# Kernel tuning notes

Hardware: AMD Instinct MI355X
Metric: run time of the kernel (lower is better)

## Reference

```python
import jax, jax.numpy as jnp
import numpy as np

K = 32  # kneighbors
BN_EPS = 1e-5


def setup_inputs() -> dict:
    key = jax.random.key(0)
    ks = jax.random.split(key, 8)
    B, N, S, C = 8, 4096, 1024, 64
    Cin = C + 6  # 70
    inp = {
        "xyz": jax.random.normal(ks[0], (B, N, 3), jnp.float32),
        "points": jax.random.normal(ks[1], (B, C, N), jnp.float32),
        "new_xyz": jax.random.normal(ks[2], (B, S, 3), jnp.float32),
        "W1": jax.random.normal(ks[3], (128, Cin), jnp.float32) / np.sqrt(Cin),
        "b1": jax.random.normal(ks[4], (128,), jnp.float32) * 0.01,
        "g1": jnp.ones((128,), jnp.float32),
        "be1": jnp.zeros((128,), jnp.float32),
        "W2": jax.random.normal(ks[5], (256, 128), jnp.float32) / np.sqrt(128),
        "b2": jax.random.normal(ks[6], (256,), jnp.float32) * 0.01,
        "g2": jnp.ones((256,), jnp.float32),
        "be2": jnp.zeros((256,), jnp.float32),
    }
    return inp


def _forward(xyz, points, new_xyz, W1, b1, g1, be1, W2, b2, g2, be2):
    B, S, _ = new_xyz.shape
    pts = jnp.transpose(points, (0, 2, 1))  # [B,N,C]
    # squared pairwise distances [B,S,N]
    sqd = (jnp.sum(new_xyz ** 2, -1)[:, :, None]
           + jnp.sum(xyz ** 2, -1)[:, None, :]
           - 2.0 * jnp.einsum('bsc,bnc->bsn', new_xyz, xyz))
    _, idx = jax.lax.top_k(-sqd, K)  # k smallest -> [B,S,K] int32
    gather = jax.vmap(lambda a, i: a[i])  # per-batch fancy gather
    gxyz = gather(xyz, idx)   # [B,S,K,3]
    gpts = gather(pts, idx)   # [B,S,K,C]
    q = jnp.broadcast_to(new_xyz[:, :, None, :], (B, S, K, 3))
    g = jnp.concatenate([gpts, gxyz, q], axis=-1)  # [B,S,K,C+6]
    x = jnp.transpose(g, (0, 3, 2, 1))  # [B,Cin,K,S]
    for W, b, gm, bt in ((W1, b1, g1, be1), (W2, b2, g2, be2)):
        x = jnp.einsum('oi,biks->boks', W, x) + b[None, :, None, None]
        mu = jnp.mean(x, axis=(0, 2, 3), keepdims=True)
        var = jnp.var(x, axis=(0, 2, 3), keepdims=True)  # biased, as torch BN train
        x = (x - mu) * jax.lax.rsqrt(var + BN_EPS)
        x = x * gm[None, :, None, None] + bt[None, :, None, None]
        x = jax.nn.relu(x)
    new_points = jnp.max(x, axis=2)  # [B,Cout,S]
    return new_xyz, new_points


def reference(xyz, points, new_xyz, W1, b1, g1, be1, W2, b2, g2, be2):
    return _forward(xyz, points, new_xyz, W1, b1, g1, be1, W2, b2, g2, be2)
```

## Files before the change

### kernel.cpp

```cpp
#include <hip/hip_runtime.h>
#include <stdint.h>

constexpr int Bn = 8, Nn = 4096, Sn = 1024, Cc = 64, KNN = 32, C1 = 128, C2 = 256;
constexpr int Qq = Bn * Sn;
constexpr int Mm = Qq * KNN;
constexpr int OUT_XYZ = Bn * Sn * 3;
constexpr float BNEPS = 1e-5f;
constexpr unsigned RSEL = 12;

constexpr size_t SZ_IDX  = (size_t)Qq * KNN * 4;
constexpr size_t SZ_PTST = (size_t)Bn * Nn * Cc * 2;
constexpr int    NB_MLP  = Mm / 64;
constexpr size_t SZ_P1   = (size_t)NB_MLP * 256 * 4;
constexpr size_t SZ_P2   = (size_t)NB_MLP * 512 * 4;
constexpr size_t OFF_IDX  = 0;
constexpr size_t OFF_PTST = OFF_IDX + SZ_IDX;
constexpr size_t OFF_P1   = OFF_PTST + SZ_PTST;
constexpr size_t OFF_P2   = OFF_P1 + SZ_P1;
constexpr size_t OFF_P1B  = OFF_P2 + SZ_P2;
constexpr size_t OFF_P2B  = OFF_P1B + (size_t)128 * 256 * 4;
constexpr size_t OFF_BN1  = OFF_P2B + (size_t)128 * 512 * 4;
constexpr size_t OFF_BN2  = OFF_BN1 + 1024;
constexpr size_t OFF_W2F  = OFF_BN2 + 2048;
constexpr size_t OFF_W1F  = OFF_W2F + (size_t)32768 * 2;
constexpr size_t OFF_Y1   = (OFF_W1F + (size_t)12288 * 2 + 255) & ~(size_t)255;
constexpr size_t OFF_MMX  = OFF_Y1 + (size_t)Mm * C1 * 2;
constexpr size_t OFF_MMN  = OFF_MMX + (size_t)Qq * C2 * 4;

typedef __attribute__((ext_vector_type(8))) __bf16 bf16x8;
typedef __attribute__((ext_vector_type(4))) float f32x4;

__device__ __forceinline__ unsigned short f2bf(float f) {
  unsigned u = __float_as_uint(f);
  u = u + 0x7FFFu + ((u >> 16) & 1u);
  return (unsigned short)(u >> 16);
}

__device__ __forceinline__ void agg_hist(unsigned* hist, unsigned bin, bool valid, int lane) {
  bool todo = valid;
  while (true) {
    unsigned long long bm = __ballot(todo);
    if (bm == 0ull) break;
    int first = __ffsll(bm) - 1;
    unsigned b = (unsigned)__shfl((int)bin, first);
    unsigned long long m = __ballot(todo && bin == b);
    if (lane == first) atomicAdd(&hist[b], (unsigned)__popcll(m));
    if (todo && bin == b) todo = false;
  }
}

__global__ __launch_bounds__(256) void k_knn(const float* __restrict__ xyz,
                                             const float* __restrict__ nxyz,
                                             int* __restrict__ idxout,
                                             const float* __restrict__ pts,
                                             const float* __restrict__ W1,
                                             const float* __restrict__ W2,
                                             unsigned short* __restrict__ ptsTbf,
                                             float* __restrict__ outdst,
                                             unsigned short* __restrict__ w1f,
                                             unsigned short* __restrict__ w2f) {
  int t = threadIdx.x;
  if (blockIdx.x >= (unsigned)Qq) {
    int blk = blockIdx.x - Qq;
    if (blk < 512) {
      __shared__ float tile[64][65];
      int b = blk >> 6, n0 = (blk & 63) * 64;
      int cl = t & 63, rw = t >> 6;
#pragma unroll
      for (int i = 0; i < 16; ++i) {
        int c = i * 4 + rw;
        tile[cl][c] = pts[((size_t)b * Cc + c) * Nn + n0 + cl];
      }
      __syncthreads();
#pragma unroll
      for (int i = 0; i < 16; ++i) {
        int nf = i * 4 + rw;
        ptsTbf[((size_t)b * Nn + n0 + nf) * Cc + cl] = f2bf(tile[nf][cl]);
      }
    } else if (blk < 608) {
      int i = t + (blk - 512) * 256;
      if (i < OUT_XYZ) outdst[i] = nxyz[i];
    } else if (blk < 656) {
      int u = t + (blk - 608) * 256;
      int j = u & 7, lane = (u >> 3) & 63, rest = u >> 9;
      int ks = rest % 3, nt = rest / 3;
      int ch = nt * 16 + (lane & 15);
      int k = ks * 32 + (lane >> 4) * 8 + j;
      w1f[u] = (k < 70) ? f2bf(W1[ch * 70 + k]) : (unsigned short)0;
    } else {
      int u = t + (blk - 656) * 256;
      int j = u & 7, lane = (u >> 3) & 63, ks = (u >> 9) & 3, ntile = u >> 11;
      int col = ntile * 16 + (lane & 15);
      int k = ks * 32 + (lane >> 4) * 8 + j;
      w2f[u] = f2bf(W2[col * C1 + k]);
    }
    return;
  }
  int q = blockIdx.x, b = q >> 10;
  int lane = t & 63, w = t >> 6;
  const float* xb = xyz + (size_t)b * Nn * 3;
  float qx = nxyz[q * 3 + 0], qy = nxyz[q * 3 + 1], qz = nxyz[q * 3 + 2];
  unsigned key[16];
  {
#pragma clang fp contract(off)
    float sqq = (qx * qx + qy * qy) + qz * qz;
#pragma unroll
    for (int i = 0; i < 16; ++i) {
      int p = t + (i << 8);
      float xl = xb[p * 3 + 0], yl = xb[p * 3 + 1], zl = xb[p * 3 + 2];
      float sqp = (xl * xl + yl * yl) + zl * zl;
      float dot = __builtin_fmaf(qz, zl, __builtin_fmaf(qy, yl, qx * xl));
      float d = (sqq + sqp) - 2.0f * dot;
      unsigned u = __float_as_uint(d);
      key[i] = (u & 0x80000000u) ? ~u : (u | 0x80000000u);
    }
  }
  __shared__ unsigned long long buf64[256];
  __shared__ unsigned hist[256];
  __shared__ unsigned hist2[256];
  __shared__ unsigned wsum[4];
  __shared__ unsigned sel_bin, sel_off, cnt, ovf, thrU, tieflag;
  __shared__ unsigned eqcnt;
  __shared__ int eqbuf[128];

  unsigned s0 = key[0], s1 = key[8];
  hist[t] = 0;
  hist2[t] = 0;
  if (t == 0) { cnt = 0; ovf = 0; thrU = 0xFFFFFFFFu; tieflag = 0; }
  __syncthreads();
  agg_hist(hist, s0 >> 24, true, lane);
  agg_hist(hist, s1 >> 24, true, lane);
  __syncthreads();
  {
    unsigned h = hist[t], v = h;
#pragma unroll
    for (int off = 1; off < 64; off <<= 1) {
      unsigned o = __shfl_up(v, off);
      if (lane >= off) v += o;
    }
    if (lane == 63) wsum[w] = v;
    __syncthreads();
    unsigned woff = 0;
    for (int ww = 0; ww < w; ++ww) woff += wsum[ww];
    v += woff;
    unsigned vex = v - h;
    if (vex < RSEL && RSEL <= v) { sel_bin = (unsigned)t; sel_off = RSEL - vex; }
    __syncthreads();
  }
  unsigned sbin = sel_bin, srem = sel_off;
  if ((s0 >> 24) == sbin) atomicAdd(&hist2[(s0 >> 16) & 255u], 1u);
  if ((s1 >> 24) == sbin) atomicAdd(&hist2[(s1 >> 16) & 255u], 1u);
  __syncthreads();
  {
    unsigned h = hist2[t], v = h;
#pragma unroll
    for (int off = 1; off < 64; off <<= 1) {
      unsigned o = __shfl_up(v, off);
      if (lane >= off) v += o;
    }
    if (lane == 63) wsum[w] = v;
    __syncthreads();
    unsigned woff = 0;
    for (int ww = 0; ww < w; ++ww) woff += wsum[ww];
    v += woff;
    unsigned vex = v - h;
    if (vex < srem && srem <= v) {
      unsigned p16 = (sbin << 8) | (unsigned)t;
      thrU = (p16 >= 0xFFFFu) ? 0xFFFFFFFFu : ((p16 + 1u) << 16);
    }
    __syncthreads();
  }
  unsigned U = thrU;
#pragma unroll
  for (int i = 0; i < 16; ++i) {
    bool take = key[i] < U;
    unsigned long long m = __ballot(take);
    if (m == 0ull) continue;
    unsigned base = 0;
    if (lane == 0) base = atomicAdd(&cnt, (unsigned)__popcll(m));
    base = (unsigned)__shfl((int)base, 0);
    if (take) {
      unsigned off = base + (unsigned)__popcll(m & ((1ull << lane) - 1ull));
      if (off < 256u)
        buf64[off] = ((unsigned long long)key[i] << 32) | (unsigned)(t + (i << 8));
      else
        ovf = 1;
    }
  }
  __syncthreads();
  unsigned ncnt = cnt;
  if (!ovf && ncnt >= (unsigned)KNN && ncnt <= 256u) {
    int nc = (int)ncnt;
    const unsigned* keyhw = reinterpret_cast<const unsigned*>(buf64);
    bool split = (nc <= 128);
    int cid = split ? (t & 127) : t;
    bool haveC = (cid < nc);
    unsigned mykey = haveC ? keyhw[2 * cid + 1] : 0xFFFFFFFFu;
    int r = 0;
    {
      int c0 = split ? (t >> 7) : 0;
      int c1 = split ? (c0 + 1) : ((nc + 63) >> 6);
      for (int c = c0; c < c1 && c * 64 < nc; ++c) {
        int ci = c * 64 + lane;
        unsigned bk = (ci < nc) ? keyhw[2 * ci + 1] : 0xFFFFFFFFu;
#pragma unroll
        for (int i = 0; i < 64; ++i) {
          unsigned ok = __builtin_amdgcn_readlane(bk, i);
          r += (ok < mykey);
        }
      }
    }
    if (split) {
      hist[t] = (unsigned)r;
      __syncthreads();
      if (t < 128) r = (int)(hist[t] + hist[t + 128]);
    }
    hist2[t] = 0;
    __syncthreads();
    bool writer = haveC && (split ? (t < 128) : true);
    if (writer) atomicAdd(&hist2[r], 1u);
    __syncthreads();
    if (hist2[t] > 1u) tieflag = 1;
    __syncthreads();
    if (tieflag) {
      unsigned long long my64 = haveC ? buf64[cid] : ~0ull;
      int rr = 0;
      int nchunk = (nc + 63) >> 6;
      for (int c = 0; c < nchunk; ++c) {
        int ci = c * 64 + lane;
        unsigned long long v = (ci < nc) ? buf64[ci] : ~0ull;
        unsigned vlo = (unsigned)v, vhi = (unsigned)(v >> 32);
#pragma unroll
        for (int i = 0; i < 64; ++i) {
          unsigned olo = __builtin_amdgcn_readlane(vlo, i);
          unsigned ohi = __builtin_amdgcn_readlane(vhi, i);
          unsigned long long o = ((unsigned long long)ohi << 32) | olo;
          rr += (o < my64);
        }
      }
      r = rr;
    }
    if (writer && r < KNN)
      idxout[q * KNN + r] = (int)(unsigned)(buf64[cid] & 0xFFFFFFFFull);
  } else {
    unsigned prefix = 0, remaining = (unsigned)KNN;
    if (t == 0) { cnt = 0; eqcnt = 0; }
#pragma unroll
    for (int shift = 24; shift >= 0; shift -= 8) {
      hist[t] = 0;
      __syncthreads();
      unsigned himask = (shift == 24) ? 0u : (0xFFFFFFFFu << ((shift + 8) & 31));
#pragma unroll
      for (int i = 0; i < 16; ++i)
        if ((key[i] & himask) == prefix)
          atomicAdd(&hist[(key[i] >> shift) & 255], 1u);
      __syncthreads();
      unsigned h = hist[t], v = h;
#pragma unroll
      for (int off = 1; off < 64; off <<= 1) {
        unsigned o = __shfl_up(v, off);
        if (lane >= off) v += o;
      }
      if (lane == 63) wsum[w] = v;
      __syncthreads();
      unsigned woff = 0;
      for (int ww = 0; ww < w; ++ww) woff += wsum[ww];
      v += woff;
      unsigned vex = v - h;
      if (vex < remaining && remaining <= v) { sel_bin = (unsigned)t; sel_off = vex; }
      __syncthreads();
      prefix |= sel_bin << shift;
      remaining -= sel_off;
    }
#pragma unroll
    for (int i = 0; i < 16; ++i) {
      int p = t + (i << 8);
      if (key[i] < prefix) {
        unsigned pos = atomicAdd(&cnt, 1u);
        idxout[q * KNN + pos] = p;
      } else if (key[i] == prefix) {
        unsigned e = atomicAdd(&eqcnt, 1u);
        if (e < 128u) eqbuf[e] = p;
      }
    }
    __syncthreads();
    if (t == 0) {
      int n = (int)min(eqcnt, 128u);
      for (int a = 1; a < n; ++a) {
        int x = eqbuf[a], bi = a - 1;
        while (bi >= 0 && eqbuf[bi] > x) { eqbuf[bi + 1] = eqbuf[bi]; --bi; }
        eqbuf[bi + 1] = x;
      }
      int base = (int)cnt;
      for (int j = 0; j < (int)remaining; ++j) idxout[q * KNN + base + j] = eqbuf[j];
    }
  }
}

__global__ __launch_bounds__(256) void k_mlp1(const unsigned short* __restrict__ ptsTbf,
                                              const float* __restrict__ xyz,
                                              const float* __restrict__ nxyz,
                                              const int* __restrict__ idx,
                                              const unsigned short* __restrict__ w1f,
                                              const float* __restrict__ b1,
                                              unsigned short* __restrict__ y1,
                                              float* __restrict__ part1) {
  __shared__ unsigned short zs[64 * 128];
  int t = threadIdx.x;
  int m0 = blockIdx.x * 64;
  int b = m0 >> 15;
  int lane = t & 63, w = t >> 6;
  bf16x8 bfrag[2][3];
  {
    const uint4* wp = reinterpret_cast<const uint4*>(w1f);
#pragma unroll
    for (int nt = 0; nt < 2; ++nt)
#pragma unroll
      for (int ks = 0; ks < 3; ++ks)
        bfrag[nt][ks] = __builtin_bit_cast(bf16x8, wp[((w * 2 + nt) * 3 + ks) * 64 + lane]);
  }
  {
    int j = t >> 2, part = t & 3;
    int m = m0 + j;
    int pid = idx[m];
    const uint4* src =
        reinterpret_cast<const uint4*>(ptsTbf + ((size_t)b * Nn + pid) * Cc + part * 16);
    char* zc = reinterpret_cast<char*>(zs);
    int base = j * 256, swz = (j & 7) << 4;
    uint4 s0 = src[0], s1 = src[1];
    *reinterpret_cast<uint4*>(zc + ((base + part * 32) ^ swz)) = s0;
    *reinterpret_cast<uint4*>(zc + ((base + part * 32 + 16) ^ swz)) = s1;
    uint4 ex = make_uint4(0u, 0u, 0u, 0u);
    if (part == 0) {
      const float* xp = xyz + ((size_t)b * Nn + pid) * 3;
      int s = (m >> 5) & (Sn - 1);
      const float* qp = nxyz + (size_t)(b * Sn + s) * 3;
      ex.x = (unsigned)f2bf(xp[0]) | ((unsigned)f2bf(xp[1]) << 16);
      ex.y = (unsigned)f2bf(xp[2]) | ((unsigned)f2bf(qp[0]) << 16);
      ex.z = (unsigned)f2bf(qp[1]) | ((unsigned)f2bf(qp[2]) << 16);
    }
    *reinterpret_cast<uint4*>(zc + ((base + (8 + part) * 16) ^ swz)) = ex;
  }
  __syncthreads();
  f32x4 acc[4][2];
#pragma unroll
  for (int mt = 0; mt < 4; ++mt)
#pragma unroll
    for (int nt = 0; nt < 2; ++nt) acc[mt][nt] = f32x4{0.f, 0.f, 0.f, 0.f};
  int r15 = lane & 15, rhi = lane >> 4;
  const char* zc = reinterpret_cast<const char*>(zs);
#pragma unroll
  for (int mt = 0; mt < 4; ++mt) {
    int row = mt * 16 + r15;
    bf16x8 af[3];
#pragma unroll
    for (int ks = 0; ks < 3; ++ks)
      af[ks] = __builtin_bit_cast(
          bf16x8, *reinterpret_cast<const uint4*>(
                      zc + ((row * 256 + ks * 64 + rhi * 16) ^ ((row & 7) << 4))));
#pragma unroll
    for (int nt = 0; nt < 2; ++nt)
#pragma unroll
      for (int ks = 0; ks < 3; ++ks)
        acc[mt][nt] =
            __builtin_amdgcn_mfma_f32_16x16x32_bf16(af[ks], bfrag[nt][ks], acc[mt][nt], 0, 0, 0);
  }
  __syncthreads();
  char* zcw = reinterpret_cast<char*>(zs);
#pragma unroll
  for (int nt = 0; nt < 2; ++nt) {
    int col = w * 32 + nt * 16 + r15;
    float bv = b1[col];
    float s = 0.f, ss = 0.f;
#pragma unroll
    for (int mt = 0; mt < 4; ++mt)
#pragma unroll
      for (int rg = 0; rg < 4; ++rg) {
        float v = acc[mt][nt][rg] + bv;
        s += v; ss += v * v;
        int row = mt * 16 + rhi * 4 + rg;
        *reinterpret_cast<unsigned short*>(zcw + ((row * 256 + col * 2) ^ ((row & 3) << 6))) =
            f2bf(v);
      }
    s += __shfl_xor(s, 16); s += __shfl_xor(s, 32);
    ss += __shfl_xor(ss, 16); ss += __shfl_xor(ss, 32);
    if (lane < 16) {
      part1[(size_t)blockIdx.x * 256 + col] = s;
      part1[(size_t)blockIdx.x * 256 + 128 + col] = ss;
    }
  }
  __syncthreads();
#pragma unroll
  for (int i = 0; i < 4; ++i) {
    int chunk = t + i * 256;
    int row = chunk >> 4, kc = chunk & 15;
    uint4 v = *reinterpret_cast<const uint4*>(
        zc + ((row * 256 + kc * 16) ^ ((row & 3) << 6)));
    *reinterpret_cast<uint4*>(y1 + (size_t)(m0 + row) * C1 + kc * 8) = v;
  }
}

__global__ __launch_bounds__(256) void k_red1a(const float* __restrict__ part1,
                                               float* __restrict__ p1b) {
  int t = threadIdx.x, r = blockIdx.x;
  float acc = 0.f;
  for (int row = r * 32; row < r * 32 + 32; ++row)
    acc += part1[(size_t)row * 256 + t];
  p1b[r * 256 + t] = acc;
}
__global__ __launch_bounds__(256) void k_red1b(const float* __restrict__ p1b,
                                               const float* __restrict__ g1,
                                               const float* __restrict__ be1,
                                               float* __restrict__ bn1) {
  __shared__ float lds[256];
  int t = threadIdx.x;
  float acc = 0.f;
  for (int row = 0; row < 128; ++row) acc += p1b[row * 256 + t];
  lds[t] = acc;
  __syncthreads();
  if (t < 128) {
    float sum = lds[t], ss = lds[128 + t];
    float mean = sum / (float)Mm;
    float var = ss / (float)Mm - mean * mean;
    float a = g1[t] * rsqrtf(var + BNEPS);
    bn1[t] = a;
    bn1[128 + t] = be1[t] - mean * a;
  }
}

__global__ __launch_bounds__(256) void k_m2(const unsigned short* __restrict__ y1,
                                            const float* __restrict__ bn1c,
                                            const unsigned short* __restrict__ w2f,
                                            const float* __restrict__ b2,
                                            float* __restrict__ part2,
                                            float* __restrict__ maxv,
                                            float* __restrict__ minv) {
  __shared__ unsigned short zs[64 * 128];
  __shared__ float bns[256];
  int t = threadIdx.x;
  int m0 = blockIdx.x * 64;
  bns[t] = bn1c[t];
  uint4 yv[4];
  const uint4* ybase = reinterpret_cast<const uint4*>(y1 + (size_t)m0 * C1);
#pragma unroll
  for (int i = 0; i < 4; ++i) yv[i] = ybase[t + i * 256];
  int lane = t & 63, w = t >> 6;
  bf16x8 bfrag[4][4];
  {
    const uint4* wp = reinterpret_cast<const uint4*>(w2f) + (size_t)(w * 4) * 4 * 64 + lane;
#pragma unroll
    for (int nt = 0; nt < 4; ++nt)
#pragma unroll
      for (int ks = 0; ks < 4; ++ks)
        bfrag[nt][ks] = __builtin_bit_cast(bf16x8, wp[(nt * 4 + ks) * 64]);
  }
  __syncthreads();
#pragma unroll
  for (int i = 0; i < 4; ++i) {
    int chunk = t + i * 256;
    int row = chunk >> 4, kc = chunk & 15;
    unsigned arr[4] = {yv[i].x, yv[i].y, yv[i].z, yv[i].w};
    unsigned zo[4];
#pragma unroll
    for (int e = 0; e < 4; ++e) {
      int c = kc * 8 + e * 2;
      float lo = __uint_as_float(arr[e] << 16);
      float hi = __uint_as_float(arr[e] & 0xFFFF0000u);
      float z0 = fmaxf(0.f, bns[c] * lo + bns[128 + c]);
      float z1 = fmaxf(0.f, bns[c + 1] * hi + bns[128 + c + 1]);
      zo[e] = (unsigned)f2bf(z0) | ((unsigned)f2bf(z1) << 16);
    }
    int byte = (row * 256 + kc * 16) ^ ((row & 7) << 4);
    *reinterpret_cast<uint4*>(reinterpret_cast<char*>(zs) + byte) =
        make_uint4(zo[0], zo[1], zo[2], zo[3]);
  }
  __syncthreads();
  f32x4 acc[4][4];
#pragma unroll
  for (int mt = 0; mt < 4; ++mt)
#pragma unroll
    for (int nt = 0; nt < 4; ++nt) acc[mt][nt] = f32x4{0.f, 0.f, 0.f, 0.f};
  int r15 = lane & 15, rhi = lane >> 4;
#pragma unroll
  for (int mt = 0; mt < 4; ++mt) {
    int row = mt * 16 + r15;
    bf16x8 af[4];
#pragma unroll
    for (int ks = 0; ks < 4; ++ks) {
      int byte = (row * 256 + ks * 64 + rhi * 16) ^ ((row & 7) << 4);
      af[ks] = __builtin_bit_cast(
          bf16x8, *reinterpret_cast<const uint4*>(reinterpret_cast<const char*>(zs) + byte));
    }
#pragma unroll
    for (int nt = 0; nt < 4; ++nt)
#pragma unroll
      for (int ks = 0; ks < 4; ++ks)
        acc[mt][nt] =
            __builtin_amdgcn_mfma_f32_16x16x32_bf16(af[ks], bfrag[nt][ks], acc[mt][nt], 0, 0, 0);
  }
  int wn0 = w * 64;
  int q0 = m0 >> 5;
#pragma unroll
  for (int nt = 0; nt < 4; ++nt) {
    int col = wn0 + nt * 16 + r15;
    float bv = b2[col];
    float s = 0.f, ss = 0.f;
    float mA = -3.0e38f, mB = -3.0e38f, nA = 3.0e38f, nB = 3.0e38f;
#pragma unroll
    for (int mt = 0; mt < 4; ++mt)
#pragma unroll
      for (int rg = 0; rg < 4; ++rg) {
        float v = acc[mt][nt][rg] + bv;
        s += v; ss += v * v;
        if (mt < 2) { mA = fmaxf(mA, v); nA = fminf(nA, v); }
        else        { mB = fmaxf(mB, v); nB = fminf(nB, v); }
      }
    s += __shfl_xor(s, 16); s += __shfl_xor(s, 32);
    ss += __shfl_xor(ss, 16); ss += __shfl_xor(ss, 32);
    mA = fmaxf(mA, __shfl_xor(mA, 16)); mA = fmaxf(mA, __shfl_xor(mA, 32));
    mB = fmaxf(mB, __shfl_xor(mB, 16)); mB = fmaxf(mB, __shfl_xor(mB, 32));
    nA = fminf(nA, __shfl_xor(nA, 16)); nA = fminf(nA, __shfl_xor(nA, 32));
    nB = fminf(nB, __shfl_xor(nB, 16)); nB = fminf(nB, __shfl_xor(nB, 32));
    if (lane < 16) {
      part2[(size_t)blockIdx.x * 512 + col] = s;
      part2[(size_t)blockIdx.x * 512 + 256 + col] = ss;
    }
    if (lane < 32) {
      int q = q0 + (lane >> 4);
      float mv = (lane < 16) ? mA : mB;
      float nv = (lane < 16) ? nA : nB;
      maxv[(size_t)q * C2 + col] = mv;
      minv[(size_t)q * C2 + col] = nv;
    }
  }
}

__global__ __launch_bounds__(512) void k_red2a(const float* __restrict__ part2,
                                               float* __restrict__ p2b) {
  int t = threadIdx.x, r = blockIdx.x;
  float acc = 0.f;
  for (int row = r * 32; row < r * 32 + 32; ++row)
    acc += part2[(size_t)row * 512 + t];
  p2b[r * 512 + t] = acc;
}
__global__ __launch_bounds__(512) void k_red2b(const float* __restrict__ p2b,
                                               const float* __restrict__ g2,
                                               const float* __restrict__ be2,
                                               float* __restrict__ bn2) {
  __shared__ float lds[512];
  int t = threadIdx.x;
  float acc = 0.f;
  for (int row = 0; row < 128; ++row) acc += p2b[row * 512 + t];
  lds[t] = acc;
  __syncthreads();
  if (t < 256) {
    float sum = lds[t], ss = lds[256 + t];
    float mean = sum / (float)Mm;
    float var = ss / (float)Mm - mean * mean;
    float a = g2[t] * rsqrtf(var + BNEPS);
    bn2[t] = a;
    bn2[256 + t] = be2[t] - mean * a;
  }
}

__global__ __launch_bounds__(256) void k_out(const float* __restrict__ maxv,
                                             const float* __restrict__ minv,
                                             const float* __restrict__ bn2,
                                             float* __restrict__ out) {
  __shared__ float tile[64][65];
  int b = blockIdx.z, col0 = blockIdx.y * 64, s0 = blockIdx.x * 64;
  int t = threadIdx.x;
  int chl = t & 63, sr = t >> 6;
  float a = bn2[col0 + chl], c = bn2[256 + col0 + chl];
  bool pos = (a >= 0.0f);
#pragma unroll
  for (int i = 0; i < 16; ++i) {
    int sl = sr * 16 + i;
    size_t q = (size_t)(b * Sn + s0 + sl);
    float v = pos ? maxv[q * C2 + col0 + chl] : minv[q * C2 + col0 + chl];
    tile[chl][sl] = fmaxf(0.f, a * v + c);
  }
  __syncthreads();
  int sl = t & 63, cr = t >> 6;
#pragma unroll
  for (int i = 0; i < 16; ++i) {
    int chl2 = i * 4 + cr;
    out[OUT_XYZ + ((size_t)(b * C2 + col0 + chl2)) * Sn + s0 + sl] = tile[chl2][sl];
  }
}

extern "C" void kernel_launch(void* const* d_in, const int* in_sizes, int n_in,
                              void* d_out, int out_size, void* d_ws, size_t ws_size,
                              hipStream_t stream) {
  (void)in_sizes; (void)n_in; (void)out_size; (void)ws_size;
  const float* xyz  = (const float*)d_in[0];
  const float* pts  = (const float*)d_in[1];
  const float* nxyz = (const float*)d_in[2];
  const float* W1   = (const float*)d_in[3];
  const float* b1   = (const float*)d_in[4];
  const float* g1   = (const float*)d_in[5];
  const float* be1  = (const float*)d_in[6];
  const float* W2   = (const float*)d_in[7];
  const float* b2   = (const float*)d_in[8];
  const float* g2   = (const float*)d_in[9];
  const float* be2  = (const float*)d_in[10];
  float* out = (float*)d_out;
  char* ws = (char*)d_ws;

  int*            idx    = (int*)(ws + OFF_IDX);
  unsigned short* ptsTbf = (unsigned short*)(ws + OFF_PTST);
  float*          part1  = (float*)(ws + OFF_P1);
  float*          part2  = (float*)(ws + OFF_P2);
  float*          p1b    = (float*)(ws + OFF_P1B);
  float*          p2b    = (float*)(ws + OFF_P2B);
  float*          bn1    = (float*)(ws + OFF_BN1);
  float*          bn2    = (float*)(ws + OFF_BN2);
  unsigned short* w2f    = (unsigned short*)(ws + OFF_W2F);
  unsigned short* w1f    = (unsigned short*)(ws + OFF_W1F);
  unsigned short* y1     = (unsigned short*)(ws + OFF_Y1);
  float*          maxv   = (float*)(ws + OFF_MMX);
  float*          minv   = (float*)(ws + OFF_MMN);

  k_knn<<<Qq + 784, 256, 0, stream>>>(xyz, nxyz, idx, pts, W1, W2, ptsTbf, out, w1f, w2f);
  k_mlp1<<<NB_MLP, 256, 0, stream>>>(ptsTbf, xyz, nxyz, idx, w1f, b1, y1, part1);
  k_red1a<<<128, 256, 0, stream>>>(part1, p1b);
  k_red1b<<<1, 256, 0, stream>>>(p1b, g1, be1, bn1);
  k_m2<<<NB_MLP, 256, 0, stream>>>(y1, bn1, w2f, b2, part2, maxv, minv);
  k_red2a<<<128, 512, 0, stream>>>(part2, p2b);
  k_red2b<<<1, 512, 0, stream>>>(p2b, g2, be2, bn2);
  k_out<<<dim3(Sn / 64, C2 / 64, Bn), 256, 0, stream>>>(maxv, minv, bn2, out);
}
```

Measured before the change: 153.8 us.

## Vectorize KNN xyz loads, store only sign-selected extremum, fold BN2 finalize into output

The KNN distance pass now reads each thread's 16 contiguous points as float4 vectors instead of strided scalar loads, which changes the point-to-thread mapping and therefore the index encoding. The second MLP kernel picks max or min per channel from the sign of gamma2 (which equals the sign of the BN scale) and writes a single value array instead of both max and min. The single-block BN2 finalize kernel is removed; each output block reduces the BN2 partial sums for its 64 channels itself. This saves a kernel launch and half the extremum traffic, at the cost of the BN2 partials being re-reduced redundantly across many output blocks.

```diff
diff --git a/kernel.cpp b/kernel.cpp
--- a/kernel.cpp
+++ b/kernel.cpp
@@ -24,8 +24,7 @@
 constexpr size_t OFF_W2F  = OFF_BN2 + 2048;
 constexpr size_t OFF_W1F  = OFF_W2F + (size_t)32768 * 2;
 constexpr size_t OFF_Y1   = (OFF_W1F + (size_t)12288 * 2 + 255) & ~(size_t)255;
-constexpr size_t OFF_MMX  = OFF_Y1 + (size_t)Mm * C1 * 2;
-constexpr size_t OFF_MMN  = OFF_MMX + (size_t)Qq * C2 * 4;
+constexpr size_t OFF_VAL  = OFF_Y1 + (size_t)Mm * C1 * 2;
 
 typedef __attribute__((ext_vector_type(8))) __bf16 bf16x8;
 typedef __attribute__((ext_vector_type(4))) float f32x4;
@@ -98,21 +97,29 @@
   }
   int q = blockIdx.x, b = q >> 10;
   int lane = t & 63, w = t >> 6;
-  const float* xb = xyz + (size_t)b * Nn * 3;
+  const float4* xb4 = reinterpret_cast<const float4*>(xyz + (size_t)b * Nn * 3);
   float qx = nxyz[q * 3 + 0], qy = nxyz[q * 3 + 1], qz = nxyz[q * 3 + 2];
   unsigned key[16];
   {
 #pragma clang fp contract(off)
     float sqq = (qx * qx + qy * qy) + qz * qz;
 #pragma unroll
-    for (int i = 0; i < 16; ++i) {
-      int p = t + (i << 8);
-      float xl = xb[p * 3 + 0], yl = xb[p * 3 + 1], zl = xb[p * 3 + 2];
-      float sqp = (xl * xl + yl * yl) + zl * zl;
-      float dot = __builtin_fmaf(qz, zl, __builtin_fmaf(qy, yl, qx * xl));
-      float d = (sqq + sqp) - 2.0f * dot;
-      unsigned u = __float_as_uint(d);
-      key[i] = (u & 0x80000000u) ? ~u : (u | 0x80000000u);
+    for (int h = 0; h < 2; ++h) {
+      float fl[24];
+#pragma unroll
+      for (int j = 0; j < 6; ++j) {
+        float4 v = xb4[t * 12 + h * 6 + j];
+        fl[4 * j + 0] = v.x; fl[4 * j + 1] = v.y; fl[4 * j + 2] = v.z; fl[4 * j + 3] = v.w;
+      }
+#pragma unroll
+      for (int i = 0; i < 8; ++i) {
+        float xl = fl[3 * i], yl = fl[3 * i + 1], zl = fl[3 * i + 2];
+        float sqp = (xl * xl + yl * yl) + zl * zl;
+        float dot = __builtin_fmaf(qz, zl, __builtin_fmaf(qy, yl, qx * xl));
+        float d = (sqq + sqp) - 2.0f * dot;
+        unsigned u = __float_as_uint(d);
+        key[h * 8 + i] = (u & 0x80000000u) ? ~u : (u | 0x80000000u);
+      }
     }
   }
   __shared__ unsigned long long buf64[256];
@@ -182,7 +189,7 @@
     if (take) {
       unsigned off = base + (unsigned)__popcll(m & ((1ull << lane) - 1ull));
       if (off < 256u)
-        buf64[off] = ((unsigned long long)key[i] << 32) | (unsigned)(t + (i << 8));
+        buf64[off] = ((unsigned long long)key[i] << 32) | (unsigned)(t * 16 + i);
       else
         ovf = 1;
     }
@@ -274,7 +281,7 @@
     }
 #pragma unroll
     for (int i = 0; i < 16; ++i) {
-      int p = t + (i << 8);
+      int p = t * 16 + i;
       if (key[i] < prefix) {
         unsigned pos = atomicAdd(&cnt, 1u);
         idxout[q * KNN + pos] = p;
@@ -432,9 +439,9 @@
                                             const float* __restrict__ bn1c,
                                             const unsigned short* __restrict__ w2f,
                                             const float* __restrict__ b2,
+                                            const float* __restrict__ g2,
                                             float* __restrict__ part2,
-                                            float* __restrict__ maxv,
-                                            float* __restrict__ minv) {
+                                            float* __restrict__ valv) {
   __shared__ unsigned short zs[64 * 128];
   __shared__ float bns[256];
   int t = threadIdx.x;
@@ -504,6 +511,7 @@
   for (int nt = 0; nt < 4; ++nt) {
     int col = wn0 + nt * 16 + r15;
     float bv = b2[col];
+    bool pos = (g2[col] >= 0.0f);
     float s = 0.f, ss = 0.f;
     float mA = -3.0e38f, mB = -3.0e38f, nA = 3.0e38f, nB = 3.0e38f;
 #pragma unroll
@@ -515,22 +523,23 @@
         if (mt < 2) { mA = fmaxf(mA, v); nA = fminf(nA, v); }
         else        { mB = fmaxf(mB, v); nB = fminf(nB, v); }
       }
+    float vA = pos ? mA : nA, vB = pos ? mB : nB;
     s += __shfl_xor(s, 16); s += __shfl_xor(s, 32);
     ss += __shfl_xor(ss, 16); ss += __shfl_xor(ss, 32);
-    mA = fmaxf(mA, __shfl_xor(mA, 16)); mA = fmaxf(mA, __shfl_xor(mA, 32));
-    mB = fmaxf(mB, __shfl_xor(mB, 16)); mB = fmaxf(mB, __shfl_xor(mB, 32));
-    nA = fminf(nA, __shfl_xor(nA, 16)); nA = fminf(nA, __shfl_xor(nA, 32));
-    nB = fminf(nB, __shfl_xor(nB, 16)); nB = fminf(nB, __shfl_xor(nB, 32));
+    if (pos) {
+      vA = fmaxf(vA, __shfl_xor(vA, 16)); vA = fmaxf(vA, __shfl_xor(vA, 32));
+      vB = fmaxf(vB, __shfl_xor(vB, 16)); vB = fmaxf(vB, __shfl_xor(vB, 32));
+    } else {
+      vA = fminf(vA, __shfl_xor(vA, 16)); vA = fminf(vA, __shfl_xor(vA, 32));
+      vB = fminf(vB, __shfl_xor(vB, 16)); vB = fminf(vB, __shfl_xor(vB, 32));
+    }
     if (lane < 16) {
       part2[(size_t)blockIdx.x * 512 + col] = s;
       part2[(size_t)blockIdx.x * 512 + 256 + col] = ss;
     }
     if (lane < 32) {
       int q = q0 + (lane >> 4);
-      float mv = (lane < 16) ? mA : mB;
-      float nv = (lane < 16) ? nA : nB;
-      maxv[(size_t)q * C2 + col] = mv;
-      minv[(size_t)q * C2 + col] = nv;
+      valv[(size_t)q * C2 + col] = (lane < 16) ? vA : vB;
     }
   }
 }
@@ -543,42 +552,47 @@
     acc += part2[(size_t)row * 512 + t];
   p2b[r * 512 + t] = acc;
 }
-__global__ __launch_bounds__(512) void k_red2b(const float* __restrict__ p2b,
-                                               const float* __restrict__ g2,
-                                               const float* __restrict__ be2,
-                                               float* __restrict__ bn2) {
-  __shared__ float lds[512];
-  int t = threadIdx.x;
-  float acc = 0.f;
-  for (int row = 0; row < 128; ++row) acc += p2b[row * 512 + t];
-  lds[t] = acc;
-  __syncthreads();
-  if (t < 256) {
-    float sum = lds[t], ss = lds[256 + t];
-    float mean = sum / (float)Mm;
-    float var = ss / (float)Mm - mean * mean;
-    float a = g2[t] * rsqrtf(var + BNEPS);
-    bn2[t] = a;
-    bn2[256 + t] = be2[t] - mean * a;
-  }
-}
-
-__global__ __launch_bounds__(256) void k_out(const float* __restrict__ maxv,
-                                             const float* __restrict__ minv,
-                                             const float* __restrict__ bn2,
+
+__global__ __launch_bounds__(256) void k_out(const float* __restrict__ valv,
+                                             const float* __restrict__ p2b,
+                                             const float* __restrict__ g2,
+                                             const float* __restrict__ be2,
                                              float* __restrict__ out) {
   __shared__ float tile[64][65];
+  __shared__ float sred[256], ssred[256];
+  __shared__ float as_[64], cs_[64];
   int b = blockIdx.z, col0 = blockIdx.y * 64, s0 = blockIdx.x * 64;
   int t = threadIdx.x;
-  int chl = t & 63, sr = t >> 6;
-  float a = bn2[col0 + chl], c = bn2[256 + col0 + chl];
-  bool pos = (a >= 0.0f);
+  int colL = t & 63, grp = t >> 6;
+  {
+    int col = col0 + colL;
+    float s = 0.f, ss = 0.f;
+    for (int row = grp * 32; row < grp * 32 + 32; ++row) {
+      s += p2b[row * 512 + col];
+      ss += p2b[row * 512 + 256 + col];
+    }
+    sred[grp * 64 + colL] = s;
+    ssred[grp * 64 + colL] = ss;
+  }
+  __syncthreads();
+  if (grp == 0) {
+    float S = sred[colL] + sred[64 + colL] + sred[128 + colL] + sred[192 + colL];
+    float SS = ssred[colL] + ssred[64 + colL] + ssred[128 + colL] + ssred[192 + colL];
+    float mean = S / (float)Mm;
+    float var = SS / (float)Mm - mean * mean;
+    float a = g2[col0 + colL] * rsqrtf(var + BNEPS);
+    as_[colL] = a;
+    cs_[colL] = be2[col0 + colL] - mean * a;
+  }
+  __syncthreads();
+  float a = as_[colL], c = cs_[colL];
+  int sr = grp;
 #pragma unroll
   for (int i = 0; i < 16; ++i) {
     int sl = sr * 16 + i;
     size_t q = (size_t)(b * Sn + s0 + sl);
-    float v = pos ? maxv[q * C2 + col0 + chl] : minv[q * C2 + col0 + chl];
-    tile[chl][sl] = fmaxf(0.f, a * v + c);
+    float v = valv[q * C2 + col0 + colL];
+    tile[colL][sl] = fmaxf(0.f, a * v + c);
   }
   __syncthreads();
   int sl = t & 63, cr = t >> 6;
@@ -614,19 +628,16 @@
   float*          p1b    = (float*)(ws + OFF_P1B);
   float*          p2b    = (float*)(ws + OFF_P2B);
   float*          bn1    = (float*)(ws + OFF_BN1);
-  float*          bn2    = (float*)(ws + OFF_BN2);
   unsigned short* w2f    = (unsigned short*)(ws + OFF_W2F);
   unsigned short* w1f    = (unsigned short*)(ws + OFF_W1F);
   unsigned short* y1     = (unsigned short*)(ws + OFF_Y1);
-  float*          maxv   = (float*)(ws + OFF_MMX);
-  float*          minv   = (float*)(ws + OFF_MMN);
+  float*          valv   = (float*)(ws + OFF_VAL);
 
   k_knn<<<Qq + 784, 256, 0, stream>>>(xyz, nxyz, idx, pts, W1, W2, ptsTbf, out, w1f, w2f);
   k_mlp1<<<NB_MLP, 256, 0, stream>>>(ptsTbf, xyz, nxyz, idx, w1f, b1, y1, part1);
   k_red1a<<<128, 256, 0, stream>>>(part1, p1b);
   k_red1b<<<1, 256, 0, stream>>>(p1b, g1, be1, bn1);
-  k_m2<<<NB_MLP, 256, 0, stream>>>(y1, bn1, w2f, b2, part2, maxv, minv);
+  k_m2<<<NB_MLP, 256, 0, stream>>>(y1, bn1, w2f, b2, g2, part2, valv);
   k_red2a<<<128, 512, 0, stream>>>(part2, p2b);
-  k_red2b<<<1, 512, 0, stream>>>(p2b, g2, be2, bn2);
-  k_out<<<dim3(Sn / 64, C2 / 64, Bn), 256, 0, stream>>>(maxv, minv, bn2, out);
-}
+  k_out<<<dim3(Sn / 64, C2 / 64, Bn), 256, 0, stream>>>(valv, p2b, g2, be2, out);
+}
```

New measurement: 140.9 us. 1.09x faster.
